# Optimization experiments

Measured on AMD Instinct MI355X. Metric: run time of the kernel, lower is better.

## Reference

```python
import jax, jax.numpy as jnp
import numpy as np

IN_FEATURES = 4096
OUT_FEATURES = 4096


def setup_inputs() -> dict:
    key = jax.random.key(0)
    k1, k2 = jax.random.split(key)
    x = jax.random.normal(k1, (4, 2048, IN_FEATURES), dtype=jnp.float32)
    latent_weight = jax.random.normal(k2, (OUT_FEATURES, IN_FEATURES), dtype=jnp.float32) * 0.02
    return {"x": x, "latent_weight": latent_weight}


def _quantize(w):
    # abs-mean scale, ternary {-alpha, 0, alpha} with threshold 0.5*alpha
    alpha = jnp.mean(jnp.abs(w))
    threshold = 0.5 * alpha
    return jnp.where(w > threshold, alpha, jnp.where(w < -threshold, -alpha, jnp.zeros_like(w)))


def reference(x, latent_weight):
    qw = _quantize(latent_weight.astype(jnp.float32))
    # F.linear: x @ qw.T  -> [B, S, out_features]
    out = jnp.einsum('bsi,oi->bso', x.astype(jnp.float32), qw)
    return out.astype(x.dtype)
```

## Files before the change

### kernel.cpp

```cpp
#include <hip/hip_runtime.h>
#include <hip/hip_bf16.h>
#include <stdint.h>

#define M_DIM 8192
#define K_DIM 4096
#define N_DIM 4096

typedef __attribute__((ext_vector_type(8))) short short8;
typedef __attribute__((ext_vector_type(4))) float f32x4;

__device__ __forceinline__ void lds_load16(const ushort* g, ushort* l) {
    __builtin_amdgcn_global_load_lds(
        (const __attribute__((address_space(1))) uint32_t*)g,
        (__attribute__((address_space(3))) uint32_t*)l, 16, 0, 0);
}

__device__ __forceinline__ ushort f2bf_rne(float f) {
    uint32_t u = __float_as_uint(f);
    uint32_t r = (u + 0x7FFFu + ((u >> 16) & 1u)) >> 16;
    return (ushort)r;
}

__global__ void k_abs_partial(const float* __restrict__ w, double* __restrict__ partial) {
    const float4* w4 = (const float4*)w;
    const int n4 = (K_DIM * N_DIM) / 4;
    double s = 0.0;
    for (int i = blockIdx.x * blockDim.x + threadIdx.x; i < n4; i += gridDim.x * blockDim.x) {
        float4 v = w4[i];
        s += (double)fabsf(v.x) + (double)fabsf(v.y) + (double)fabsf(v.z) + (double)fabsf(v.w);
    }
    #pragma unroll
    for (int off = 32; off > 0; off >>= 1) s += __shfl_down(s, off, 64);
    __shared__ double sm[4];
    int lane = threadIdx.x & 63, wv = threadIdx.x >> 6;
    if (lane == 0) sm[wv] = s;
    __syncthreads();
    if (threadIdx.x == 0) partial[blockIdx.x] = sm[0] + sm[1] + sm[2] + sm[3];
}

__global__ void k_alpha(const double* __restrict__ partial, float* __restrict__ alpha_out) {
    double s = 0.0;
    for (int i = threadIdx.x; i < 1024; i += 256) s += partial[i];
    #pragma unroll
    for (int off = 32; off > 0; off >>= 1) s += __shfl_down(s, off, 64);
    __shared__ double sm[4];
    int lane = threadIdx.x & 63, wv = threadIdx.x >> 6;
    if (lane == 0) sm[wv] = s;
    __syncthreads();
    if (threadIdx.x == 0) {
        double total = sm[0] + sm[1] + sm[2] + sm[3];
        alpha_out[0] = (float)(total * (1.0 / 16777216.0));
    }
}

__global__ void k_quant(const float* __restrict__ w, const float* __restrict__ alpha_p,
                        ushort* __restrict__ qw) {
    const float thr = 0.5f * alpha_p[0];
    int i = blockIdx.x * blockDim.x + threadIdx.x;
    float4 v = ((const float4*)w)[i];
    ushort4 q;
    q.x = v.x > thr ? 0x3F80 : (v.x < -thr ? 0xBF80 : 0);
    q.y = v.y > thr ? 0x3F80 : (v.y < -thr ? 0xBF80 : 0);
    q.z = v.z > thr ? 0x3F80 : (v.z < -thr ? 0xBF80 : 0);
    q.w = v.w > thr ? 0x3F80 : (v.w < -thr ? 0xBF80 : 0);
    ((ushort4*)qw)[i] = q;
}

__global__ void k_cast(const float* __restrict__ x, ushort* __restrict__ xb) {
    int i = blockIdx.x * blockDim.x + threadIdx.x;
    float4 v = ((const float4*)x)[i];
    ushort4 o;
    o.x = f2bf_rne(v.x);
    o.y = f2bf_rne(v.y);
    o.z = f2bf_rne(v.z);
    o.w = f2bf_rne(v.w);
    ((ushort4*)xb)[i] = o;
}

#define BM 128
#define BN 128
#define BK 64

__global__ __launch_bounds__(256, 2) void k_gemm(const ushort* __restrict__ A,
                                                 const ushort* __restrict__ B,
                                                 const float* __restrict__ alpha_p,
                                                 float* __restrict__ C) {
    __shared__ __align__(16) ushort sA[BM * BK];
    __shared__ __align__(16) ushort sB[BN * BK];

    const int tid = threadIdx.x;
    const int lane = tid & 63;
    const int bm = blockIdx.y, bn = blockIdx.x;
    const int wv = tid >> 6;
    const int wm = (wv & 1) * 64;
    const int wn = (wv >> 1) * 64;

    f32x4 acc[4][4] = {};

    const ushort* Abase = A + (size_t)(bm * BM) * K_DIM;
    const ushort* Bbase = B + (size_t)(bn * BN) * K_DIM;

    const int r = lane & 15, q = lane >> 4;

    for (int kb = 0; kb < K_DIM / BK; ++kb) {
        const int k0 = kb * BK;
        #pragma unroll
        for (int j = 0; j < 4; ++j) {
            int c = j * 256 + tid;
            int row = c >> 3, kc = (c & 7) * 8;
            lds_load16(Abase + (size_t)row * K_DIM + k0 + kc, &sA[c * 8]);
            lds_load16(Bbase + (size_t)row * K_DIM + k0 + kc, &sB[c * 8]);
        }
        __syncthreads();

        #pragma unroll
        for (int kk = 0; kk < BK; kk += 32) {
            short8 af[4], bfr[4];
            #pragma unroll
            for (int i = 0; i < 4; ++i)
                af[i] = *(const short8*)&sA[(wm + i * 16 + r) * BK + kk + q * 8];
            #pragma unroll
            for (int j = 0; j < 4; ++j)
                bfr[j] = *(const short8*)&sB[(wn + j * 16 + r) * BK + kk + q * 8];
            #pragma unroll
            for (int i = 0; i < 4; ++i)
                #pragma unroll
                for (int j = 0; j < 4; ++j)
                    acc[i][j] = __builtin_amdgcn_mfma_f32_16x16x32_bf16(af[i], bfr[j], acc[i][j], 0, 0, 0);
        }
        __syncthreads();
    }

    const float alpha = alpha_p[0];
    #pragma unroll
    for (int i = 0; i < 4; ++i)
        #pragma unroll
        for (int j = 0; j < 4; ++j)
            #pragma unroll
            for (int v = 0; v < 4; ++v) {
                int row = bm * BM + wm + i * 16 + q * 4 + v;
                int col = bn * BN + wn + j * 16 + r;
                C[(size_t)row * N_DIM + col] = alpha * acc[i][j][v];
            }
}

extern "C" void kernel_launch(void* const* d_in, const int* in_sizes, int n_in,
                              void* d_out, int out_size, void* d_ws, size_t ws_size,
                              hipStream_t stream) {
    const float* x = (const float*)d_in[0];
    const float* w = (const float*)d_in[1];
    float* out = (float*)d_out;

    char* ws = (char*)d_ws;
    double* partial = (double*)ws;
    float* alpha = (float*)(ws + 8192);
    ushort* qw = (ushort*)(ws + 16384);
    ushort* xb = (ushort*)(ws + 16384 + (size_t)K_DIM * N_DIM * 2);

    k_abs_partial<<<1024, 256, 0, stream>>>(w, partial);
    k_alpha<<<1, 256, 0, stream>>>(partial, alpha);
    k_quant<<<(K_DIM * N_DIM / 4) / 256, 256, 0, stream>>>(w, alpha, qw);
    k_cast<<<(M_DIM * K_DIM / 4) / 256, 256, 0, stream>>>(x, xb);

    dim3 grid(N_DIM / BN, M_DIM / BM);
    k_gemm<<<grid, dim3(256), 0, stream>>>(xb, qw, alpha, out);
}
```

Measured before the change: 547.3 us.

## Rewrite GEMM as 256x256 tile, 8-wave, double-buffered pipelined kernel with swizzled LDS

```diff
diff --git a/kernel.cpp b/kernel.cpp
--- a/kernel.cpp
+++ b/kernel.cpp
@@ -77,71 +77,157 @@
     ((ushort4*)xb)[i] = o;
 }
 
-#define BM 128
-#define BN 128
-#define BK 64
-
-__global__ __launch_bounds__(256, 2) void k_gemm(const ushort* __restrict__ A,
+#define NT (K_DIM / 64)
+
+#define MFMA16(a, b, c) __builtin_amdgcn_mfma_f32_16x16x32_bf16((a), (b), (c), 0, 0, 0)
+
+__global__ __launch_bounds__(512, 2) void k_gemm(const ushort* __restrict__ A,
                                                  const ushort* __restrict__ B,
                                                  const float* __restrict__ alpha_p,
                                                  float* __restrict__ C) {
-    __shared__ __align__(16) ushort sA[BM * BK];
-    __shared__ __align__(16) ushort sB[BN * BK];
+    __shared__ __align__(16) ushort lds[65536];
 
     const int tid = threadIdx.x;
     const int lane = tid & 63;
-    const int bm = blockIdx.y, bn = blockIdx.x;
-    const int wv = tid >> 6;
-    const int wm = (wv & 1) * 64;
-    const int wn = (wv >> 1) * 64;
-
-    f32x4 acc[4][4] = {};
-
-    const ushort* Abase = A + (size_t)(bm * BM) * K_DIM;
-    const ushort* Bbase = B + (size_t)(bn * BN) * K_DIM;
-
+    const int w = tid >> 6;
+    const int wr = w >> 2;
+    const int wc = w & 3;
     const int r = lane & 15, q = lane >> 4;
 
-    for (int kb = 0; kb < K_DIM / BK; ++kb) {
-        const int k0 = kb * BK;
-        #pragma unroll
-        for (int j = 0; j < 4; ++j) {
-            int c = j * 256 + tid;
-            int row = c >> 3, kc = (c & 7) * 8;
-            lds_load16(Abase + (size_t)row * K_DIM + k0 + kc, &sA[c * 8]);
-            lds_load16(Bbase + (size_t)row * K_DIM + k0 + kc, &sB[c * 8]);
-        }
-        __syncthreads();
-
-        #pragma unroll
-        for (int kk = 0; kk < BK; kk += 32) {
-            short8 af[4], bfr[4];
-            #pragma unroll
-            for (int i = 0; i < 4; ++i)
-                af[i] = *(const short8*)&sA[(wm + i * 16 + r) * BK + kk + q * 8];
-            #pragma unroll
-            for (int j = 0; j < 4; ++j)
-                bfr[j] = *(const short8*)&sB[(wn + j * 16 + r) * BK + kk + q * 8];
-            #pragma unroll
-            for (int i = 0; i < 4; ++i)
-                #pragma unroll
-                for (int j = 0; j < 4; ++j)
-                    acc[i][j] = __builtin_amdgcn_mfma_f32_16x16x32_bf16(af[i], bfr[j], acc[i][j], 0, 0, 0);
-        }
-        __syncthreads();
+    const int wg = blockIdx.x;
+    const int swz = (wg & 7) * 64 + (wg >> 3);
+    const int bm = swz >> 4;
+    const int bn = swz & 15;
+
+    float alpha = alpha_p[0];
+    asm volatile("" :: "v"(alpha));
+
+    const ushort* Abase = A + (size_t)bm * 256 * K_DIM;
+    const ushort* Bbase = B + (size_t)bn * 256 * K_DIM;
+
+    const int srow = tid >> 3;
+    const int sch = (tid & 7) ^ (srow & 7);
+
+    const int ch0 = q ^ (r & 7);
+    const int o0 = r * 64 + ch0 * 8;
+    const int o1 = r * 64 + (ch0 ^ 4) * 8;
+
+    f32x4 acc[8][4] = {};
+
+    auto SA = [&](int h, int bb, int tt) {
+        const ushort* g = Abase + (size_t)(h * 128 + srow) * K_DIM + tt * 64 + sch * 8;
+        ushort* l = lds + bb * 32768 + h * 8192 + tid * 8;
+        lds_load16(g, l);
+        lds_load16(g + (size_t)64 * K_DIM, l + 4096);
+    };
+    auto SB = [&](int h, int bb, int tt) {
+        const ushort* g = Bbase + (size_t)(h * 128 + srow) * K_DIM + tt * 64 + sch * 8;
+        ushort* l = lds + bb * 32768 + 16384 + h * 8192 + tid * 8;
+        lds_load16(g, l);
+        lds_load16(g + (size_t)64 * K_DIM, l + 4096);
+    };
+
+    SA(0, 0, 0); SA(1, 0, 0); SB(0, 0, 0); SB(1, 0, 0);
+    SB(0, 1, 1); SB(1, 1, 1);
+    asm volatile("s_waitcnt vmcnt(4)" ::: "memory");
+    __builtin_amdgcn_s_barrier();
+
+    for (int t = 0; t < NT; ++t) {
+        const int b = t & 1;
+        const ushort* aL = lds + b * 32768 + wr * 8192;
+        const ushort* bL = lds + b * 32768 + 16384 + (wc >> 1) * 8192 + (wc & 1) * 4096;
+        short8 am[4][2], b01[2][2], b23[2][2];
+
+        #pragma unroll
+        for (int i = 0; i < 4; ++i) {
+            am[i][0] = *(const short8*)(aL + i * 1024 + o0);
+            am[i][1] = *(const short8*)(aL + i * 1024 + o1);
+        }
+        #pragma unroll
+        for (int j = 0; j < 2; ++j) {
+            b01[j][0] = *(const short8*)(bL + j * 1024 + o0);
+            b01[j][1] = *(const short8*)(bL + j * 1024 + o1);
+        }
+        if (t + 1 < NT) SA(0, (t + 1) & 1, t + 1);
+        __builtin_amdgcn_s_barrier();
+        asm volatile("s_waitcnt lgkmcnt(0)" ::: "memory");
+        __builtin_amdgcn_sched_barrier(0);
+        __builtin_amdgcn_s_setprio(1);
+        #pragma unroll
+        for (int i = 0; i < 4; ++i)
+            #pragma unroll
+            for (int j = 0; j < 2; ++j) {
+                acc[i][j] = MFMA16(am[i][0], b01[j][0], acc[i][j]);
+                acc[i][j] = MFMA16(am[i][1], b01[j][1], acc[i][j]);
+            }
+        __builtin_amdgcn_s_setprio(0);
+        __builtin_amdgcn_s_barrier();
+
+        #pragma unroll
+        for (int j = 0; j < 2; ++j) {
+            b23[j][0] = *(const short8*)(bL + (2 + j) * 1024 + o0);
+            b23[j][1] = *(const short8*)(bL + (2 + j) * 1024 + o1);
+        }
+        if (t + 1 < NT) SA(1, (t + 1) & 1, t + 1);
+        __builtin_amdgcn_s_barrier();
+        asm volatile("s_waitcnt lgkmcnt(0)" ::: "memory");
+        __builtin_amdgcn_sched_barrier(0);
+        __builtin_amdgcn_s_setprio(1);
+        #pragma unroll
+        for (int i = 0; i < 4; ++i)
+            #pragma unroll
+            for (int j = 0; j < 2; ++j) {
+                acc[i][2 + j] = MFMA16(am[i][0], b23[j][0], acc[i][2 + j]);
+                acc[i][2 + j] = MFMA16(am[i][1], b23[j][1], acc[i][2 + j]);
+            }
+        __builtin_amdgcn_s_setprio(0);
+        __builtin_amdgcn_s_barrier();
+
+        #pragma unroll
+        for (int i = 0; i < 4; ++i) {
+            am[i][0] = *(const short8*)(aL + (4 + i) * 1024 + o0);
+            am[i][1] = *(const short8*)(aL + (4 + i) * 1024 + o1);
+        }
+        if (t + 2 < NT) SB(0, b, t + 2);
+        __builtin_amdgcn_s_barrier();
+        asm volatile("s_waitcnt lgkmcnt(0)" ::: "memory");
+        __builtin_amdgcn_sched_barrier(0);
+        __builtin_amdgcn_s_setprio(1);
+        #pragma unroll
+        for (int i = 0; i < 4; ++i)
+            #pragma unroll
+            for (int j = 0; j < 2; ++j) {
+                acc[4 + i][2 + j] = MFMA16(am[i][0], b23[j][0], acc[4 + i][2 + j]);
+                acc[4 + i][2 + j] = MFMA16(am[i][1], b23[j][1], acc[4 + i][2 + j]);
+            }
+        __builtin_amdgcn_s_setprio(0);
+        __builtin_amdgcn_s_barrier();
+
+        if (t + 2 < NT) SB(1, b, t + 2);
+        __builtin_amdgcn_s_barrier();
+        __builtin_amdgcn_s_setprio(1);
+        #pragma unroll
+        for (int i = 0; i < 4; ++i)
+            #pragma unroll
+            for (int j = 0; j < 2; ++j) {
+                acc[4 + i][j] = MFMA16(am[i][0], b01[j][0], acc[4 + i][j]);
+                acc[4 + i][j] = MFMA16(am[i][1], b01[j][1], acc[4 + i][j]);
+            }
+        __builtin_amdgcn_s_setprio(0);
+        if (t + 2 < NT)       asm volatile("s_waitcnt vmcnt(4)" ::: "memory");
+        else if (t + 2 == NT) asm volatile("s_waitcnt vmcnt(0)" ::: "memory");
+        __builtin_amdgcn_s_barrier();
     }
 
-    const float alpha = alpha_p[0];
+    const int row0 = bm * 256 + wr * 128 + q * 4;
+    const int col0 = bn * 256 + wc * 64 + r;
     #pragma unroll
-    for (int i = 0; i < 4; ++i)
+    for (int i = 0; i < 8; ++i)
         #pragma unroll
         for (int j = 0; j < 4; ++j)
             #pragma unroll
-            for (int v = 0; v < 4; ++v) {
-                int row = bm * BM + wm + i * 16 + q * 4 + v;
-                int col = bn * BN + wn + j * 16 + r;
-                C[(size_t)row * N_DIM + col] = alpha * acc[i][j][v];
-            }
+            for (int v = 0; v < 4; ++v)
+                C[(size_t)(row0 + i * 16 + v) * N_DIM + col0 + j * 16] = alpha * acc[i][j][v];
 }
 
 extern "C" void kernel_launch(void* const* d_in, const int* in_sizes, int n_in,
@@ -162,6 +248,5 @@
     k_quant<<<(K_DIM * N_DIM / 4) / 256, 256, 0, stream>>>(w, alpha, qw);
     k_cast<<<(M_DIM * K_DIM / 4) / 256, 256, 0, stream>>>(x, xb);
 
-    dim3 grid(N_DIM / BN, M_DIM / BM);
-    k_gemm<<<grid, dim3(256), 0, stream>>>(xb, qw, alpha, out);
-}
+    k_gemm<<<512, 512, 0, stream>>>(xb, qw, alpha, out);
+}
```

New measurement: 490.2 us. 10.4% less time.
